# Kernel tuning notes

Hardware: AMD Instinct MI355X
Metric: run time of the kernel (lower is better)

## Reference

```python
import jax, jax.numpy as jnp
import numpy as np

NOISE_RATIO = 25
NORM_TERM = 9.0

def setup_inputs() -> dict:
    key = jax.random.key(0)
    k1, k2, k3, k4, k5 = jax.random.split(key, 5)
    N, E, V, K = 4096, 1024, 50257, NOISE_RATIO
    x = jax.random.normal(k1, (N, E), dtype=jnp.float32)
    target = jax.random.randint(k2, (N,), 0, V)
    noise_idx = jax.random.randint(k3, (N, K), 0, V)
    # decoder params per IndexLinear.reset_parameters: weight ~ U(-0.1, 0.1), bias = 0
    weight = jax.random.uniform(k4, (V, E), dtype=jnp.float32, minval=-0.1, maxval=0.1)
    bias = jnp.zeros((V,), dtype=jnp.float32)
    # noise distribution over the vocab (positive, normalized)
    noise = jax.random.uniform(k5, (V,), dtype=jnp.float32, minval=0.1, maxval=1.0)
    noise = noise / jnp.sum(noise)
    return {"x": x, "target": target, "noise_idx": noise_idx,
            "weight": weight, "bias": bias, "noise": noise}

def reference(x, target, noise_idx, weight, bias, noise):
    """NCE loss (training branch), size_average=True.
    x: (N, E), target: (N,), noise_idx: (N, K), weight: (V, E), bias: (V,), noise: (V,)
    """
    N = x.shape[0]
    k = jnp.float32(NOISE_RATIO)
    # IndexLinear: gather rows for [target | noise] then per-sample (1,E)@(E,1+K)
    idx = jnp.concatenate([target[:, None], noise_idx], axis=1)   # (N, 1+K)
    w_rows = weight[idx]                                          # (N, 1+K, E)
    b_rows = bias[idx]                                            # (N, 1+K)
    logits = b_rows + jnp.einsum('ne,nke->nk', x, w_rows)         # (N, 1+K)
    probs = jnp.exp(logits - NORM_TERM)
    data_prob = probs[:, 0]                                       # (N,)
    noise_in_data = probs[:, 1:]                                  # (N, K)
    pn_target = noise[target]                                     # (N,)
    pn_noise = noise[noise_idx]                                   # (N, K)
    rnn_loss = jnp.log(data_prob / (data_prob + k * pn_target))
    noise_loss = jnp.sum(jnp.log(k * pn_noise / (noise_in_data + k * pn_noise)), axis=1)
    loss = -jnp.sum(rnn_loss + noise_loss)
    return loss / N
```

## Files before the change

### kernel.cpp

```cpp
#include <hip/hip_runtime.h>
#include <hip/hip_bf16.h>


#define NN 4096
#define EE 1024
#define KK 25
#define NBUCKET 256

__device__ __forceinline__ void fma4(float4& a, const float4& p, const float4& q) {
    a.x += p.x * q.x; a.y += p.y * q.y; a.z += p.z * q.z; a.w += p.w * q.w;
}

__global__ __launch_bounds__(256) void nce_main_kernel(
    const float* __restrict__ x,
    const int* __restrict__ target,
    const int* __restrict__ noise_idx,
    const float* __restrict__ weight,
    const float* __restrict__ bias,
    const float* __restrict__ noise,
    float* __restrict__ buckets)
{
    const int n = blockIdx.x;
    const int wave = threadIdx.x >> 6;
    const int lane = threadIdx.x & 63;

    const int nj = (wave < 2) ? 7 : 6;

    int rows[7];
#pragma unroll
    for (int jj = 0; jj < 7; ++jj) {
        const int j = wave + (jj << 2);
        rows[jj] = (jj < nj) ? ((j == 0) ? target[n] : noise_idx[n * KK + (j - 1)])
                             : 0;
    }

    const float4* x4 = (const float4*)(x + (size_t)n * EE);
    float4 xr[4];
#pragma unroll
    for (int p = 0; p < 4; ++p) xr[p] = x4[p * 64 + lane];

    float4 wr[7][4];
#pragma unroll
    for (int jj = 0; jj < 7; ++jj) {
        const float4* w4 = (const float4*)(weight + (size_t)rows[jj] * EE);
#pragma unroll
        for (int p = 0; p < 4; ++p) wr[jj][p] = w4[p * 64 + lane];
    }

    float sacc[7];
#pragma unroll
    for (int jj = 0; jj < 7; ++jj) {
        float4 a = make_float4(0.f, 0.f, 0.f, 0.f);
#pragma unroll
        for (int p = 0; p < 4; ++p) fma4(a, xr[p], wr[jj][p]);
        sacc[jj] = (a.x + a.y) + (a.z + a.w);
    }

#pragma unroll
    for (int jj = 0; jj < 7; ++jj) {
#pragma unroll
        for (int off = 32; off > 0; off >>= 1)
            sacc[jj] += __shfl_xor(sacc[jj], off);
    }

    if (lane == 0) {
        float part = 0.0f;
#pragma unroll
        for (int jj = 0; jj < 7; ++jj) {
            if (jj < nj) {
                const int j = wave + (jj << 2);
                const int row = rows[jj];
                const float logit = sacc[jj] + bias[row];
                const float p = expf(logit - 9.0f);
                const float pn25 = 25.0f * noise[row];
                part += (j == 0) ? logf(p / (p + pn25))
                                 : logf(pn25 / (p + pn25));
            }
        }
        atomicAdd(&buckets[(n + wave * 64) & (NBUCKET - 1)], -part);
    }
}

__global__ __launch_bounds__(64) void nce_finalize_kernel(
    const float* __restrict__ buckets, float* __restrict__ out)
{
    float acc = buckets[threadIdx.x] + buckets[threadIdx.x + 64]
              + buckets[threadIdx.x + 128] + buckets[threadIdx.x + 192];
#pragma unroll
    for (int off = 32; off > 0; off >>= 1)
        acc += __shfl_xor(acc, off);
    if (threadIdx.x == 0)
        out[0] = acc / (float)NN;
}

extern "C" void kernel_launch(void* const* d_in, const int* in_sizes, int n_in,
                              void* d_out, int out_size, void* d_ws, size_t ws_size,
                              hipStream_t stream) {
    const float* x        = (const float*)d_in[0];
    const int*   target   = (const int*)d_in[1];
    const int*   noiseIdx = (const int*)d_in[2];
    const float* weight   = (const float*)d_in[3];
    const float* bias     = (const float*)d_in[4];
    const float* noise    = (const float*)d_in[5];
    float* out = (float*)d_out;
    float* buckets = (float*)d_ws;

    hipMemsetAsync(buckets, 0, NBUCKET * sizeof(float), stream);
    nce_main_kernel<<<NN, 256, 0, stream>>>(x, target, noiseIdx, weight, bias, noise, buckets);
    nce_finalize_kernel<<<1, 64, 0, stream>>>(buckets, out);
}
```

Baseline: 313.9 us.

## Split sample rows across eight waves and reduce block partials in shared memory

```diff
diff --git a/kernel.cpp b/kernel.cpp
--- a/kernel.cpp
+++ b/kernel.cpp
@@ -1,5 +1,4 @@
 #include <hip/hip_runtime.h>
-#include <hip/hip_bf16.h>
 
 
 #define NN 4096
@@ -11,7 +10,7 @@
     a.x += p.x * q.x; a.y += p.y * q.y; a.z += p.z * q.z; a.w += p.w * q.w;
 }
 
-__global__ __launch_bounds__(256) void nce_main_kernel(
+__global__ __launch_bounds__(512, 4) void nce_main_kernel(
     const float* __restrict__ x,
     const int* __restrict__ target,
     const int* __restrict__ noise_idx,
@@ -23,61 +22,89 @@
     const int n = blockIdx.x;
     const int wave = threadIdx.x >> 6;
     const int lane = threadIdx.x & 63;
+    const int nj = (wave < 2) ? 4 : 3;
 
-    const int nj = (wave < 2) ? 7 : 6;
-
-    int rows[7];
+    int rows[4];
 #pragma unroll
-    for (int jj = 0; jj < 7; ++jj) {
-        const int j = wave + (jj << 2);
+    for (int jj = 0; jj < 4; ++jj) {
+        const int j = wave + (jj << 3);
         rows[jj] = (jj < nj) ? ((j == 0) ? target[n] : noise_idx[n * KK + (j - 1)])
                              : 0;
+    }
+    float bv[4], nv[4];
+#pragma unroll
+    for (int jj = 0; jj < 4; ++jj) {
+        bv[jj] = bias[rows[jj]];
+        nv[jj] = noise[rows[jj]];
     }
 
     const float4* x4 = (const float4*)(x + (size_t)n * EE);
     float4 xr[4];
 #pragma unroll
-    for (int p = 0; p < 4; ++p) xr[p] = x4[p * 64 + lane];
+    for (int p = 0; p < 4; ++p) xr[p] = x4[(p << 6) + lane];
 
-    float4 wr[7][4];
+    float4 wr[4][4];
 #pragma unroll
-    for (int jj = 0; jj < 7; ++jj) {
+    for (int jj = 0; jj < 3; ++jj) {
         const float4* w4 = (const float4*)(weight + (size_t)rows[jj] * EE);
 #pragma unroll
-        for (int p = 0; p < 4; ++p) wr[jj][p] = w4[p * 64 + lane];
+        for (int p = 0; p < 4; ++p) wr[jj][p] = w4[(p << 6) + lane];
+    }
+    if (nj == 4) {
+        const float4* w4 = (const float4*)(weight + (size_t)rows[3] * EE);
+#pragma unroll
+        for (int p = 0; p < 4; ++p) wr[3][p] = w4[(p << 6) + lane];
     }
 
-    float sacc[7];
+    float sacc[4];
 #pragma unroll
-    for (int jj = 0; jj < 7; ++jj) {
+    for (int jj = 0; jj < 3; ++jj) {
         float4 a = make_float4(0.f, 0.f, 0.f, 0.f);
 #pragma unroll
         for (int p = 0; p < 4; ++p) fma4(a, xr[p], wr[jj][p]);
         sacc[jj] = (a.x + a.y) + (a.z + a.w);
     }
+    sacc[3] = 0.f;
+    if (nj == 4) {
+        float4 a = make_float4(0.f, 0.f, 0.f, 0.f);
+#pragma unroll
+        for (int p = 0; p < 4; ++p) fma4(a, xr[p], wr[3][p]);
+        sacc[3] = (a.x + a.y) + (a.z + a.w);
+    }
 
 #pragma unroll
-    for (int jj = 0; jj < 7; ++jj) {
+    for (int jj = 0; jj < 3; ++jj) {
 #pragma unroll
         for (int off = 32; off > 0; off >>= 1)
             sacc[jj] += __shfl_xor(sacc[jj], off);
     }
+    if (nj == 4) {
+#pragma unroll
+        for (int off = 32; off > 0; off >>= 1)
+            sacc[3] += __shfl_xor(sacc[3], off);
+    }
 
+    __shared__ float wpart[8];
     if (lane == 0) {
         float part = 0.0f;
 #pragma unroll
-        for (int jj = 0; jj < 7; ++jj) {
+        for (int jj = 0; jj < 4; ++jj) {
             if (jj < nj) {
-                const int j = wave + (jj << 2);
-                const int row = rows[jj];
-                const float logit = sacc[jj] + bias[row];
+                const float logit = sacc[jj] + bv[jj];
                 const float p = expf(logit - 9.0f);
-                const float pn25 = 25.0f * noise[row];
-                part += (j == 0) ? logf(p / (p + pn25))
-                                 : logf(pn25 / (p + pn25));
+                const float pn25 = 25.0f * nv[jj];
+                part += (wave == 0 && jj == 0) ? logf(p / (p + pn25))
+                                               : logf(pn25 / (p + pn25));
             }
         }
-        atomicAdd(&buckets[(n + wave * 64) & (NBUCKET - 1)], -part);
+        wpart[wave] = part;
+    }
+    __syncthreads();
+    if (threadIdx.x == 0) {
+        float t = 0.f;
+#pragma unroll
+        for (int w = 0; w < 8; ++w) t += wpart[w];
+        atomicAdd(&buckets[n & (NBUCKET - 1)], -t);
     }
 }
 
@@ -106,6 +133,6 @@
     float* buckets = (float*)d_ws;
 
     hipMemsetAsync(buckets, 0, NBUCKET * sizeof(float), stream);
-    nce_main_kernel<<<NN, 256, 0, stream>>>(x, target, noiseIdx, weight, bias, noise, buckets);
+    nce_main_kernel<<<NN, 512, 0, stream>>>(x, target, noiseIdx, weight, bias, noise, buckets);
     nce_finalize_kernel<<<1, 64, 0, stream>>>(buckets, out);
 }
```

After: 310.4 us (median of 2 runs). About the same (-1.1%).
